# Kernel optimization log

Measured on AMD Instinct MI355X. Metric: run time of the kernel, lower is better.

## Reference

```python
import jax, jax.numpy as jnp
import numpy as np

N_PLAYERS, N_POS, N_TEAMS = 200000, 320, 32
FEAT, EMB, HID = 128, 64, 128
E_P2P, E_P2T, E_CHEM = 400000, 640, 1000000
NUM_ROUNDS = 3


def _linear(x, w, b):
    return x @ w + b


def _attention(emb, edges, q_w, q_b, k_w, k_b, v_w, v_b):
    # chemistry attention: softmax over ALL edges (dim=0 in the torch code)
    src, dst = edges[0], edges[1]
    Q = _linear(emb[dst], q_w, q_b)          # (E, EMB)
    K = _linear(emb[src], k_w, k_b)
    V = _linear(emb[src], v_w, v_b)
    scores = (Q * K).sum(axis=1) / jnp.asarray(EMB ** 0.5, emb.dtype)  # (E,)
    attn = jax.nn.softmax(scores)            # global softmax across edges
    messages = attn[:, None] * V             # (E, EMB)
    agg = jax.ops.segment_sum(messages, dst, num_segments=emb.shape[0])
    return emb + agg


def _message_pass(src_emb, dst_emb, edges, msg_w, msg_b, upd_w, upd_b):
    src, dst = edges[0], edges[1]
    messages = jax.nn.relu(_linear(src_emb[src], msg_w, msg_b))  # (E, EMB)
    n_dst = dst_emb.shape[0]
    agg = jax.ops.segment_sum(messages, dst, num_segments=n_dst)
    counts = jax.ops.segment_sum(jnp.ones((edges.shape[1],), src_emb.dtype), dst, num_segments=n_dst)
    agg = agg / jnp.clip(counts, 1.0)[:, None]  # mean aggregation
    h = jnp.concatenate([dst_emb, agg], axis=1)  # (n_dst, 2*EMB)
    return jax.nn.relu(_linear(h, upd_w, upd_b))


def setup_inputs() -> dict:
    key = jax.random.key(0)
    ks = jax.random.split(key, 32)
    g = lambda k, shape, fan_in: jax.random.normal(k, shape, jnp.float32) / np.sqrt(fan_in)
    inp = {}
    inp['player_features'] = jax.random.normal(ks[0], (N_PLAYERS, FEAT), jnp.float32)
    inp['position_indices'] = jax.random.randint(ks[1], (N_POS,), 0, 10, jnp.int32)
    inp['team_indices'] = jnp.arange(N_TEAMS, dtype=jnp.int32)
    inp['p2p_edges'] = jnp.stack([
        jax.random.randint(ks[2], (E_P2P,), 0, N_PLAYERS, jnp.int32),
        jax.random.randint(ks[3], (E_P2P,), 0, N_POS, jnp.int32)])
    inp['p2t_edges'] = jnp.stack([
        jax.random.randint(ks[4], (E_P2T,), 0, N_POS, jnp.int32),
        jax.random.randint(ks[5], (E_P2T,), 0, N_TEAMS, jnp.int32)])
    inp['chem_edges'] = jax.random.randint(ks[6], (2, E_CHEM), 0, N_PLAYERS, jnp.int32)
    inp['home_team_idx'] = 0
    inp['away_team_idx'] = 1
    # player encoder
    inp['enc_w1'] = g(ks[7], (FEAT, HID), FEAT); inp['enc_b1'] = jnp.zeros((HID,), jnp.float32)
    inp['enc_w2'] = g(ks[8], (HID, EMB), HID); inp['enc_b2'] = jnp.zeros((EMB,), jnp.float32)
    # embedding tables
    inp['pos_emb_table'] = jax.random.normal(ks[9], (10, EMB), jnp.float32)
    inp['team_emb_table'] = jax.random.normal(ks[10], (32, EMB), jnp.float32)
    # chemistry attention
    for name, k in (('q', ks[11]), ('k', ks[12]), ('v', ks[13])):
        inp[name + '_w'] = g(k, (EMB, EMB), EMB); inp[name + '_b'] = jnp.zeros((EMB,), jnp.float32)
    # message passing layers
    inp['p2p_msg_w'] = g(ks[14], (EMB, EMB), EMB); inp['p2p_msg_b'] = jnp.zeros((EMB,), jnp.float32)
    inp['p2p_upd_w'] = g(ks[15], (2 * EMB, EMB), 2 * EMB); inp['p2p_upd_b'] = jnp.zeros((EMB,), jnp.float32)
    inp['p2t_msg_w'] = g(ks[16], (EMB, EMB), EMB); inp['p2t_msg_b'] = jnp.zeros((EMB,), jnp.float32)
    inp['p2t_upd_w'] = g(ks[17], (2 * EMB, EMB), 2 * EMB); inp['p2t_upd_b'] = jnp.zeros((EMB,), jnp.float32)
    # game predictor
    inp['gp_w1'] = g(ks[18], (2 * EMB, HID), 2 * EMB); inp['gp_b1'] = jnp.zeros((HID,), jnp.float32)
    inp['gp_w2'] = g(ks[19], (HID, 64), HID); inp['gp_b2'] = jnp.zeros((64,), jnp.float32)
    inp['gp_w3'] = g(ks[20], (64, 1), 64); inp['gp_b3'] = jnp.zeros((1,), jnp.float32)
    return inp


def reference(player_features, position_indices, team_indices, p2p_edges, p2t_edges,
              chem_edges, home_team_idx, away_team_idx,
              enc_w1, enc_b1, enc_w2, enc_b2, pos_emb_table, team_emb_table,
              q_w, q_b, k_w, k_b, v_w, v_b,
              p2p_msg_w, p2p_msg_b, p2p_upd_w, p2p_upd_b,
              p2t_msg_w, p2t_msg_b, p2t_upd_w, p2t_upd_b,
              gp_w1, gp_b1, gp_w2, gp_b2, gp_w3, gp_b3):
    # player encoder (dropout omitted: eval mode)
    h = jax.nn.relu(_linear(player_features, enc_w1, enc_b1))
    player_embeds = _linear(h, enc_w2, enc_b2)  # (N_PLAYERS, EMB)
    player_embeds = _attention(player_embeds, chem_edges, q_w, q_b, k_w, k_b, v_w, v_b)
    position_embeds = pos_emb_table[position_indices]  # (N_POS, EMB)
    for _ in range(NUM_ROUNDS):
        position_embeds = _message_pass(player_embeds, position_embeds, p2p_edges,
                                        p2p_msg_w, p2p_msg_b, p2p_upd_w, p2p_upd_b)
    team_embeds = team_emb_table[team_indices]  # (N_TEAMS, EMB)
    for _ in range(NUM_ROUNDS):
        team_embeds = _message_pass(position_embeds, team_embeds, p2t_edges,
                                    p2t_msg_w, p2t_msg_b, p2t_upd_w, p2t_upd_b)
    game_embed = jnp.concatenate([team_embeds[home_team_idx], team_embeds[away_team_idx]])  # (2*EMB,)
    z = jax.nn.relu(_linear(game_embed, gp_w1, gp_b1))
    z = jax.nn.relu(_linear(z, gp_w2, gp_b2))
    logit = _linear(z, gp_w3, gp_b3)  # (1,)
    return jax.nn.sigmoid(logit)
```

## Files before the change

### kernel.cpp

```cpp
#include <hip/hip_runtime.h>
#include <hip/hip_bf16.h>

#define NP     200000
#define NPOS   320
#define NT     32
#define FEAT   128
#define EMB    64
#define HID    128
#define EP2P   400000
#define EP2T   640
#define ECHEM  1000000

#define CHEM_CAP 32
#define P2P_CAP  2048
#define T2_CAP   64
#define SC_GRID  2048
#define PB_BLOCKS 64
#define AGG_SPLIT 8

typedef unsigned short u16;
typedef __attribute__((ext_vector_type(8))) short short8;
typedef __attribute__((ext_vector_type(4))) float f32x4;

static __device__ inline u16 f2bf(float f) {
    unsigned u = __float_as_uint(f);
    return (u16)((u + 0x7fffu + ((u >> 16) & 1u)) >> 16);
}
static __device__ inline float bf2f(u16 h) {
    return __uint_as_float(((unsigned)h) << 16);
}
static __device__ inline float bprod(unsigned a, unsigned b) {
    float a0 = __uint_as_float(a << 16), a1 = __uint_as_float(a & 0xffff0000u);
    float b0 = __uint_as_float(b << 16), b1 = __uint_as_float(b & 0xffff0000u);
    return fmaf(a0, b0, a1 * b1);
}

__global__ __launch_bounds__(256) void init_kernel(int* __restrict__ chem_cnt,
                                                   int* __restrict__ p2p_cnt,
                                                   float* __restrict__ Zp,
                                                   const int* __restrict__ pos_idx,
                                                   const float* __restrict__ pos_table,
                                                   float* __restrict__ pos0,
                                                   float* __restrict__ pos_agg,
                                                   const float* __restrict__ w1,
                                                   const float* __restrict__ w2,
                                                   const float* __restrict__ qw,
                                                   const float* __restrict__ kw,
                                                   const float* __restrict__ vw,
                                                   const float* __restrict__ mw,
                                                   u16* __restrict__ Wpack)
{
    int t = blockIdx.x * 256 + threadIdx.x;
    if (t < NP) chem_cnt[t] = 0;
    if (t < NPOS) p2p_cnt[t] = 0;
    if (t < NPOS * EMB) {
        pos0[t] = pos_table[pos_idx[t >> 6] * EMB + (t & 63)];
        pos_agg[t] = 0.f;
    }
    if (t == 0) *Zp = 0.f;
    if (t < 40960) {
        float v;
        if (t < 16384)        { int i = t;         v = w1[(i & 127) * 128 + (i >> 7)]; }
        else if (t < 24576)   { int i = t - 16384; v = w2[(i & 127) * 64  + (i >> 7)]; }
        else if (t < 28672)   { int i = t - 24576; v = qw[(i & 63) * 64 + (i >> 6)]; }
        else if (t < 32768)   { int i = t - 28672; v = kw[(i & 63) * 64 + (i >> 6)]; }
        else if (t < 36864)   { int i = t - 32768; v = vw[(i & 63) * 64 + (i >> 6)]; }
        else                  { int i = t - 36864; v = mw[(i & 63) * 64 + (i >> 6)]; }
        Wpack[t] = f2bf(v);
    }
}

__global__ __launch_bounds__(256) void mfma_enc(
    const float* __restrict__ X,
    const u16* __restrict__ W1t, const u16* __restrict__ W2t,
    const u16* __restrict__ Qt,  const u16* __restrict__ Kt, const u16* __restrict__ Vt,
    const float* __restrict__ b1, const float* __restrict__ b2,
    const float* __restrict__ qbv, const float* __restrict__ kbv, const float* __restrict__ vbv,
    float* __restrict__ emb,
    u16* __restrict__ Qb, u16* __restrict__ Kb, u16* __restrict__ Vb)
{
    __shared__ u16 hb[4][16 * 136];
    __shared__ u16 eb[4][16 * 72];
    const int tid = threadIdx.x, wave = tid >> 6, lane = tid & 63;
    const int m_ = lane & 15, quad = lane >> 4;
    const int rbase = blockIdx.x * 64 + wave * 16;

    const float4* xrow = (const float4*)(X + (size_t)(rbase + m_) * 128);
    short8 ax[4];
#pragma unroll
    for (int kk = 0; kk < 4; ++kk) {
        float4 u = xrow[kk * 8 + quad * 2];
        float4 v = xrow[kk * 8 + quad * 2 + 1];
        short8 t;
        t[0] = (short)f2bf(u.x); t[1] = (short)f2bf(u.y);
        t[2] = (short)f2bf(u.z); t[3] = (short)f2bf(u.w);
        t[4] = (short)f2bf(v.x); t[5] = (short)f2bf(v.y);
        t[6] = (short)f2bf(v.z); t[7] = (short)f2bf(v.w);
        ax[kk] = t;
    }

    u16* hrow = &hb[wave][0];
#pragma unroll
    for (int n0 = 0; n0 < 8; ++n0) {
        float bv = b1[n0 * 16 + m_];
        f32x4 acc = {bv, bv, bv, bv};
        const short8* w = (const short8*)(W1t + (size_t)(n0 * 16 + m_) * 128);
#pragma unroll
        for (int kk = 0; kk < 4; ++kk)
            acc = __builtin_amdgcn_mfma_f32_16x16x32_bf16(ax[kk], w[kk * 4 + quad], acc, 0, 0, 0);
#pragma unroll
        for (int r = 0; r < 4; ++r)
            hrow[(quad * 4 + r) * 136 + n0 * 16 + m_] = f2bf(fmaxf(acc[r], 0.f));
    }

    short8 ah[4];
#pragma unroll
    for (int kk = 0; kk < 4; ++kk)
        ah[kk] = *(const short8*)&hrow[m_ * 136 + kk * 32 + quad * 8];

    u16* erow = &eb[wave][0];
#pragma unroll
    for (int n0 = 0; n0 < 4; ++n0) {
        float bv = b2[n0 * 16 + m_];
        f32x4 acc = {bv, bv, bv, bv};
        const short8* w = (const short8*)(W2t + (size_t)(n0 * 16 + m_) * 128);
#pragma unroll
        for (int kk = 0; kk < 4; ++kk)
            acc = __builtin_amdgcn_mfma_f32_16x16x32_bf16(ah[kk], w[kk * 4 + quad], acc, 0, 0, 0);
#pragma unroll
        for (int r = 0; r < 4; ++r) {
            float v = acc[r];
            emb[(size_t)(rbase + quad * 4 + r) * 64 + n0 * 16 + m_] = v;
            erow[(quad * 4 + r) * 72 + n0 * 16 + m_] = f2bf(v);
        }
    }

    short8 ae[2];
#pragma unroll
    for (int kk = 0; kk < 2; ++kk)
        ae[kk] = *(const short8*)&erow[m_ * 72 + kk * 32 + quad * 8];

    const u16*   Wt3[3] = {Qt, Kt, Vt};
    const float* Bb3[3] = {qbv, kbv, vbv};
    u16*         Ob3[3] = {Qb, Kb, Vb};
#pragma unroll
    for (int m3 = 0; m3 < 3; ++m3) {
        const u16* Wt = Wt3[m3];
        const float* bp = Bb3[m3];
        u16* O = Ob3[m3];
#pragma unroll
        for (int n0 = 0; n0 < 4; ++n0) {
            float bv = bp[n0 * 16 + m_];
            f32x4 acc = {bv, bv, bv, bv};
            const short8* w = (const short8*)(Wt + (size_t)(n0 * 16 + m_) * 64);
#pragma unroll
            for (int kk = 0; kk < 2; ++kk)
                acc = __builtin_amdgcn_mfma_f32_16x16x32_bf16(ae[kk], w[kk * 4 + quad], acc, 0, 0, 0);
#pragma unroll
            for (int r = 0; r < 4; ++r)
                O[(size_t)(rbase + quad * 4 + r) * 64 + n0 * 16 + m_] = f2bf(acc[r]);
        }
    }
}

__global__ __launch_bounds__(256) void chem_attn(const u16* __restrict__ Qb,
                                                 const u16* __restrict__ Kb,
                                                 const int* __restrict__ chem,
                                                 int* __restrict__ cnt,
                                                 uint2* __restrict__ swlist,
                                                 float* __restrict__ Zp)
{
    __shared__ float wsum[4];
    int tid = threadIdx.x;
    int lane = tid & 63, wave = tid >> 6;
    float zsum = 0.f;
    for (int e = blockIdx.x * 256 + tid; e < ECHEM; e += SC_GRID * 256) {
        int src = chem[e];
        int dst = chem[ECHEM + e];
        const uint4* q = (const uint4*)(Qb + (size_t)dst * 64);
        const uint4* k = (const uint4*)(Kb + (size_t)src * 64);
        uint4 qv[8], kv[8];
#pragma unroll
        for (int i = 0; i < 8; ++i) qv[i] = q[i];
#pragma unroll
        for (int i = 0; i < 8; ++i) kv[i] = k[i];
        float p = 0.f;
#pragma unroll
        for (int i = 0; i < 8; ++i)
            p += bprod(qv[i].x, kv[i].x) + bprod(qv[i].y, kv[i].y)
               + bprod(qv[i].z, kv[i].z) + bprod(qv[i].w, kv[i].w);
        float w = __expf(p * 0.125f);
        zsum += w;
        int pos = atomicAdd(&cnt[dst], 1);
        if (pos < CHEM_CAP)
            swlist[dst * CHEM_CAP + pos] = make_uint2((unsigned)src, __float_as_uint(w));
    }
    for (int off = 1; off < 64; off <<= 1) zsum += __shfl_xor(zsum, off);
    if (lane == 0) wsum[wave] = zsum;
    __syncthreads();
    if (tid == 0) atomicAdd(Zp, wsum[0] + wsum[1] + wsum[2] + wsum[3]);
}

__global__ __launch_bounds__(256) void chem_agg_msg(const float* __restrict__ emb,
                                                    const u16* __restrict__ Vb,
                                                    const int* __restrict__ cnt,
                                                    const uint2* __restrict__ swlist,
                                                    const float* __restrict__ Zp,
                                                    const u16* __restrict__ Msgt,
                                                    const float* __restrict__ mb,
                                                    u16* __restrict__ Mpb)
{
    __shared__ u16 eb[4][16 * 72];
    const int tid = threadIdx.x, wave = tid >> 6, lane = tid & 63;
    const int m_ = lane & 15, quad = lane >> 4;
    const int d0 = blockIdx.x * 64 + wave * 16;
    const int srow = lane >> 3, scol = (lane & 7) * 8;
    const float invZ = 1.f / Zp[0];
    u16* erow = &eb[wave][0];
#pragma unroll 1
    for (int t = 0; t < 16; ++t) {
        int d = d0 + t;
        float base = emb[(size_t)d * 64 + lane];
        int c = cnt[d]; if (c > CHEM_CAP) c = CHEM_CAP;
        int sv = 0; float wv = 0.f;
        if (lane < c) {
            uint2 p = swlist[d * CHEM_CAP + lane];
            sv = (int)p.x; wv = __uint_as_float(p.y);
        }
        float acc = 0.f;
        int i = 0;
        for (; i + 4 <= c; i += 4) {
            int s0 = __shfl(sv, i),     s1 = __shfl(sv, i + 1);
            int s2 = __shfl(sv, i + 2), s3 = __shfl(sv, i + 3);
            float w0 = __shfl(wv, i),     w1 = __shfl(wv, i + 1);
            float w2 = __shfl(wv, i + 2), w3 = __shfl(wv, i + 3);
            float v0 = bf2f(Vb[(size_t)s0 * 64 + lane]);
            float v1 = bf2f(Vb[(size_t)s1 * 64 + lane]);
            float v2 = bf2f(Vb[(size_t)s2 * 64 + lane]);
            float v3 = bf2f(Vb[(size_t)s3 * 64 + lane]);
            acc += w0 * v0 + w1 * v1 + w2 * v2 + w3 * v3;
        }
        for (; i < c; ++i) {
            int s = __shfl(sv, i);
            float w = __shfl(wv, i);
            acc += w * bf2f(Vb[(size_t)s * 64 + lane]);
        }
        erow[t * 72 + lane] = f2bf(base + acc * invZ);
    }
    short8 a0 = *(const short8*)&erow[m_ * 72 + quad * 8];
    short8 a1 = *(const short8*)&erow[m_ * 72 + 32 + quad * 8];
#pragma unroll
    for (int n0 = 0; n0 < 4; ++n0) {
        float bv = mb[n0 * 16 + m_];
        f32x4 acc = {bv, bv, bv, bv};
        const short8* w = (const short8*)(Msgt + (size_t)(n0 * 16 + m_) * 64);
        acc = __builtin_amdgcn_mfma_f32_16x16x32_bf16(a0, w[quad], acc, 0, 0, 0);
        acc = __builtin_amdgcn_mfma_f32_16x16x32_bf16(a1, w[4 + quad], acc, 0, 0, 0);
#pragma unroll
        for (int r = 0; r < 4; ++r)
            erow[(quad * 4 + r) * 72 + n0 * 16 + m_] = f2bf(fmaxf(acc[r], 0.f));
    }
    short8 r0 = *(const short8*)&erow[srow * 72 + scol];
    short8 r1 = *(const short8*)&erow[(srow + 8) * 72 + scol];
    *(short8*)(Mpb + (size_t)(d0 + srow) * 64 + scol) = r0;
    *(short8*)(Mpb + (size_t)(d0 + 8 + srow) * 64 + scol) = r1;
}

__global__ __launch_bounds__(256) void p2p_bucket(const int* __restrict__ p2p,
                                                  int* __restrict__ cnt,
                                                  int* __restrict__ list)
{
    __shared__ int lhist[NPOS];
    __shared__ int lbase[NPOS];
    int tid = threadIdx.x;
    for (int i = tid; i < NPOS; i += 256) lhist[i] = 0;
    __syncthreads();
    const int chunk = (EP2P + PB_BLOCKS - 1) / PB_BLOCKS;
    int e0 = blockIdx.x * chunk;
    int e1 = e0 + chunk; if (e1 > EP2P) e1 = EP2P;
    for (int e = e0 + tid; e < e1; e += 256)
        atomicAdd(&lhist[p2p[EP2P + e]], 1);
    __syncthreads();
    for (int i = tid; i < NPOS; i += 256) {
        lbase[i] = atomicAdd(&cnt[i], lhist[i]);
        lhist[i] = 0;
    }
    __syncthreads();
    for (int e = e0 + tid; e < e1; e += 256) {
        int d = p2p[EP2P + e];
        int p = lbase[d] + atomicAdd(&lhist[d], 1);
        if (p < P2P_CAP) list[d * P2P_CAP + p] = p2p[e];
    }
}

__global__ __launch_bounds__(256) void p2p_agg(const u16* __restrict__ Mpb,
                                               const int* __restrict__ cnt,
                                               const int* __restrict__ list,
                                               float* __restrict__ pos_agg)
{
    __shared__ float part[4 * 64];
    int d = blockIdx.x >> 3;
    int sp = blockIdx.x & (AGG_SPLIT - 1);
    int wave = threadIdx.x >> 6, lane = threadIdx.x & 63;
    int c = cnt[d];
    int cl = c > P2P_CAP ? P2P_CAP : c;
    int seg = (cl + AGG_SPLIT - 1) / AGG_SPLIT;
    int i0b = sp * seg;
    int i1 = i0b + seg; if (i1 > cl) i1 = cl;
    float acc = 0.f;
    for (int i0 = i0b + wave * 64; i0 < i1; i0 += 256) {
        int n = i1 - i0; if (n > 64) n = 64;
        int sv = (lane < n) ? list[d * P2P_CAP + i0 + lane] : 0;
        int i = 0;
        for (; i + 4 <= n; i += 4) {
            int s0 = __shfl(sv, i),     s1 = __shfl(sv, i + 1);
            int s2 = __shfl(sv, i + 2), s3 = __shfl(sv, i + 3);
            float v0 = bf2f(Mpb[(size_t)s0 * 64 + lane]);
            float v1 = bf2f(Mpb[(size_t)s1 * 64 + lane]);
            float v2 = bf2f(Mpb[(size_t)s2 * 64 + lane]);
            float v3 = bf2f(Mpb[(size_t)s3 * 64 + lane]);
            acc += v0 + v1 + v2 + v3;
        }
        for (; i < n; ++i) {
            int s = __shfl(sv, i);
            acc += bf2f(Mpb[(size_t)s * 64 + lane]);
        }
    }
    part[wave * 64 + lane] = acc;
    __syncthreads();
    if (wave == 0) {
        float t = part[lane] + part[64 + lane] + part[128 + lane] + part[192 + lane];
        atomicAdd(&pos_agg[d * 64 + lane], t);
    }
}

__global__ __launch_bounds__(256) void pos_rounds(const float* __restrict__ pos0,
                                                  const float* __restrict__ agg,
                                                  const int* __restrict__ cnt,
                                                  const float* __restrict__ upd_w,
                                                  const float* __restrict__ upd_b,
                                                  const float* __restrict__ msg_w,
                                                  const float* __restrict__ msg_b,
                                                  float* __restrict__ Mt)
{
    __shared__ float cur[4][64], nxt[4][64], aggw[4][64];
    int tid = threadIdx.x;
    int r = tid >> 6, j = tid & 63;
    int row = blockIdx.x * 4 + r;
    int c = cnt[row];
    float invc = 1.f / (float)(c < 1 ? 1 : c);
    float aw = 0.f;
    const float* ar = agg + row * 64;
#pragma unroll 8
    for (int k = 0; k < 64; ++k) aw += ar[k] * upd_w[(64 + k) * 64 + j];
    aggw[r][j] = aw * invc + upd_b[j];
    cur[r][j] = pos0[row * 64 + j];
    __syncthreads();
#pragma unroll 1
    for (int round = 0; round < 3; ++round) {
        float acc = aggw[r][j];
#pragma unroll 8
        for (int k = 0; k < 64; ++k) acc += cur[r][k] * upd_w[k * 64 + j];
        nxt[r][j] = fmaxf(acc, 0.f);
        __syncthreads();
        cur[r][j] = nxt[r][j];
        __syncthreads();
    }
    float acc = msg_b[j];
#pragma unroll 8
    for (int k = 0; k < 64; ++k) acc += cur[r][k] * msg_w[k * 64 + j];
    Mt[row * 64 + j] = fmaxf(acc, 0.f);
}

__global__ __launch_bounds__(256) void p2t_head(
    const float* __restrict__ Mt,
    const int* __restrict__ p2t_edges,
    const float* __restrict__ upd_w, const float* __restrict__ upd_b,
    const int* __restrict__ team_indices,
    const float* __restrict__ team_table,
    const int* __restrict__ home_p, const int* __restrict__ away_p,
    const float* __restrict__ gp_w1, const float* __restrict__ gp_b1,
    const float* __restrict__ gp_w2, const float* __restrict__ gp_b2,
    const float* __restrict__ gp_w3, const float* __restrict__ gp_b3,
    float* __restrict__ out)
{
    __shared__ int   tcnt[NT];
    __shared__ int   tlist[NT * T2_CAP];
    __shared__ float aggbar[NT * 64];
    __shared__ float teamA[NT * 64];
    __shared__ float teamB[NT * 64];
    __shared__ float z1[128];
    __shared__ float z2[64];
    int tid = threadIdx.x;

    if (tid < NT) tcnt[tid] = 0;
    __syncthreads();
    for (int e = tid; e < EP2T; e += 256) {
        int s = p2t_edges[e], d = p2t_edges[EP2T + e];
        int p = atomicAdd(&tcnt[d], 1);
        if (p < T2_CAP) tlist[d * T2_CAP + p] = s;
    }
    __syncthreads();
    for (int i = tid; i < NT * 64; i += 256) {
        int d = i >> 6, c = i & 63;
        int cn = tcnt[d];
        int cl = cn > T2_CAP ? T2_CAP : cn;
        float acc = 0.f;
        for (int j = 0; j < cl; ++j) acc += Mt[tlist[d * T2_CAP + j] * 64 + c];
        float dv = cn < 1 ? 1.f : (float)cn;
        aggbar[i] = acc / dv;
        teamA[i] = team_table[team_indices[d] * 64 + c];
    }
    __syncthreads();

    float* tin = teamA; float* tout = teamB;
    for (int round = 0; round < 3; ++round) {
        for (int i = tid; i < NT * 64; i += 256) {
            int r = i >> 6, j = i & 63;
            float acc = upd_b[j];
            for (int k = 0; k < 64; ++k) acc += tin[r * 64 + k] * upd_w[k * 64 + j];
            for (int k = 0; k < 64; ++k) acc += aggbar[r * 64 + k] * upd_w[(64 + k) * 64 + j];
            tout[i] = fmaxf(acc, 0.f);
        }
        __syncthreads();
        float* tmp = tin; tin = tout; tout = tmp;
    }

    int home = home_p[0], away = away_p[0];
    if (tid < 128) {
        float acc = gp_b1[tid];
        for (int k = 0; k < 128; ++k) {
            float g = (k < 64) ? tin[home * 64 + k] : tin[away * 64 + (k - 64)];
            acc += g * gp_w1[k * 128 + tid];
        }
        z1[tid] = fmaxf(acc, 0.f);
    }
    __syncthreads();
    if (tid < 64) {
        float acc = gp_b2[tid];
        for (int k = 0; k < 128; ++k) acc += z1[k] * gp_w2[k * 64 + tid];
        z2[tid] = fmaxf(acc, 0.f);
    }
    __syncthreads();
    if (tid == 0) {
        float acc = gp_b3[0];
        for (int k = 0; k < 64; ++k) acc += z2[k] * gp_w3[k];
        out[0] = 1.f / (1.f + __expf(-acc));
    }
}

extern "C" void kernel_launch(void* const* d_in, const int* in_sizes, int n_in,
                              void* d_out, int out_size, void* d_ws, size_t ws_size,
                              hipStream_t stream)
{
    const float* X        = (const float*)d_in[0];
    const int*   pos_idx  = (const int*)d_in[1];
    const int*   team_idx = (const int*)d_in[2];
    const int*   p2p      = (const int*)d_in[3];
    const int*   p2t      = (const int*)d_in[4];
    const int*   chem     = (const int*)d_in[5];
    const int*   home_p   = (const int*)d_in[6];
    const int*   away_p   = (const int*)d_in[7];
    const float* enc_w1   = (const float*)d_in[8];
    const float* enc_b1   = (const float*)d_in[9];
    const float* enc_w2   = (const float*)d_in[10];
    const float* enc_b2   = (const float*)d_in[11];
    const float* pos_tab  = (const float*)d_in[12];
    const float* team_tab = (const float*)d_in[13];
    const float* q_w = (const float*)d_in[14]; const float* q_b = (const float*)d_in[15];
    const float* k_w = (const float*)d_in[16]; const float* k_b = (const float*)d_in[17];
    const float* v_w = (const float*)d_in[18]; const float* v_b = (const float*)d_in[19];
    const float* p2p_msg_w = (const float*)d_in[20]; const float* p2p_msg_b = (const float*)d_in[21];
    const float* p2p_upd_w = (const float*)d_in[22]; const float* p2p_upd_b = (const float*)d_in[23];
    const float* p2t_msg_w = (const float*)d_in[24]; const float* p2t_msg_b = (const float*)d_in[25];
    const float* p2t_upd_w = (const float*)d_in[26]; const float* p2t_upd_b = (const float*)d_in[27];
    const float* gp_w1 = (const float*)d_in[28]; const float* gp_b1 = (const float*)d_in[29];
    const float* gp_w2 = (const float*)d_in[30]; const float* gp_b2 = (const float*)d_in[31];
    const float* gp_w3 = (const float*)d_in[32]; const float* gp_b3 = (const float*)d_in[33];
    float* out = (float*)d_out;

    char* ws = (char*)d_ws;
    uint2*    swlist    = (uint2*)(ws + 0);
    float*    emb       = (float*)(ws + 51200000);
    u16*      Qb        = (u16*)  (ws + 102400000);
    u16*      Kb        = (u16*)  (ws + 128000000);
    u16*      Vb        = (u16*)  (ws + 153600000);
    u16*      Mpb       = (u16*)  (ws + 179200000);
    int*      p2p_list  = (int*)  (ws + 204800000);
    int*      chem_cnt  = (int*)  (ws + 207421440);
    int*      p2p_cnt   = (int*)  (ws + 208221440);
    float*    pos_agg   = (float*)(ws + 208222720);
    float*    posA      = (float*)(ws + 208304640);
    float*    Mt        = (float*)(ws + 208386560);
    float*    Zp        = (float*)(ws + 208468480);
    u16*      Wpack     = (u16*)  (ws + 208468496);
    u16* W1t  = Wpack;
    u16* W2t  = Wpack + 16384;
    u16* Qt   = Wpack + 24576;
    u16* Kt   = Wpack + 28672;
    u16* Vt   = Wpack + 32768;
    u16* Msgt = Wpack + 36864;

    const int NB_NP = (NP + 255) / 256;

    hipLaunchKernelGGL(init_kernel, dim3(NB_NP), dim3(256), 0, stream,
                       chem_cnt, p2p_cnt, Zp, pos_idx, pos_tab, posA, pos_agg,
                       enc_w1, enc_w2, q_w, k_w, v_w, p2p_msg_w, Wpack);
    hipLaunchKernelGGL(mfma_enc, dim3(NP / 64), dim3(256), 0, stream,
                       X, W1t, W2t, Qt, Kt, Vt,
                       enc_b1, enc_b2, q_b, k_b, v_b,
                       emb, Qb, Kb, Vb);
    hipLaunchKernelGGL(chem_attn, dim3(SC_GRID), dim3(256), 0, stream,
                       Qb, Kb, chem, chem_cnt, swlist, Zp);
    hipLaunchKernelGGL(chem_agg_msg, dim3(NP / 64), dim3(256), 0, stream,
                       emb, Vb, chem_cnt, swlist, Zp, Msgt, p2p_msg_b, Mpb);
    hipLaunchKernelGGL(p2p_bucket, dim3(PB_BLOCKS), dim3(256), 0, stream, p2p, p2p_cnt, p2p_list);
    hipLaunchKernelGGL(p2p_agg, dim3(NPOS * AGG_SPLIT), dim3(256), 0, stream,
                       Mpb, p2p_cnt, p2p_list, pos_agg);
    hipLaunchKernelGGL(pos_rounds, dim3(NPOS / 4), dim3(256), 0, stream,
                       posA, pos_agg, p2p_cnt, p2p_upd_w, p2p_upd_b,
                       p2t_msg_w, p2t_msg_b, Mt);
    hipLaunchKernelGGL(p2t_head, dim3(1), dim3(256), 0, stream,
                       Mt, p2t, p2t_upd_w, p2t_upd_b, team_idx, team_tab, home_p, away_p,
                       gp_w1, gp_b1, gp_w2, gp_b2, gp_w3, gp_b3, out);
}
```

Baseline: 619.6 us.

## Restructure chemistry attention into dst-bucketed gather with fused unnormalized aggregation

Chemistry edges are now bucketed by destination in a separate pass before the encoder. A per-destination wave kernel then computes the Q·K scores, the exp weights and the weighted V sum in one gather, writing an unnormalized aggregate and a per-node partition sum. A small reduction kernel produces the global softmax denominator, and the final message kernel only rescales. The encoder also becomes a persistent grid-stride kernel that prefetches the next chunk's inputs into registers. This avoids writing and re-reading weighted edge lists and the per-edge scattered K loads, at the cost of extra kernel launches, wider per-lane gathers and a bf16 rounding of the intermediate aggregate.

```diff
diff --git a/kernel.cpp b/kernel.cpp
--- a/kernel.cpp
+++ b/kernel.cpp
@@ -17,6 +17,8 @@
 #define SC_GRID  2048
 #define PB_BLOCKS 64
 #define AGG_SPLIT 8
+#define ENC_GRID 1024
+#define NCHUNK   (NP / 64)
 
 typedef unsigned short u16;
 typedef __attribute__((ext_vector_type(8))) short short8;
@@ -28,11 +30,6 @@
 }
 static __device__ inline float bf2f(u16 h) {
     return __uint_as_float(((unsigned)h) << 16);
-}
-static __device__ inline float bprod(unsigned a, unsigned b) {
-    float a0 = __uint_as_float(a << 16), a1 = __uint_as_float(a & 0xffff0000u);
-    float b0 = __uint_as_float(b << 16), b1 = __uint_as_float(b & 0xffff0000u);
-    return fmaf(a0, b0, a1 * b1);
 }
 
 __global__ __launch_bounds__(256) void init_kernel(int* __restrict__ chem_cnt,
@@ -83,128 +80,194 @@
     __shared__ u16 eb[4][16 * 72];
     const int tid = threadIdx.x, wave = tid >> 6, lane = tid & 63;
     const int m_ = lane & 15, quad = lane >> 4;
-    const int rbase = blockIdx.x * 64 + wave * 16;
-
-    const float4* xrow = (const float4*)(X + (size_t)(rbase + m_) * 128);
-    short8 ax[4];
-#pragma unroll
-    for (int kk = 0; kk < 4; ++kk) {
-        float4 u = xrow[kk * 8 + quad * 2];
-        float4 v = xrow[kk * 8 + quad * 2 + 1];
-        short8 t;
-        t[0] = (short)f2bf(u.x); t[1] = (short)f2bf(u.y);
-        t[2] = (short)f2bf(u.z); t[3] = (short)f2bf(u.w);
-        t[4] = (short)f2bf(v.x); t[5] = (short)f2bf(v.y);
-        t[6] = (short)f2bf(v.z); t[7] = (short)f2bf(v.w);
-        ax[kk] = t;
-    }
-
-    u16* hrow = &hb[wave][0];
-#pragma unroll
-    for (int n0 = 0; n0 < 8; ++n0) {
-        float bv = b1[n0 * 16 + m_];
-        f32x4 acc = {bv, bv, bv, bv};
-        const short8* w = (const short8*)(W1t + (size_t)(n0 * 16 + m_) * 128);
+
+    int chunk = blockIdx.x;
+    if (chunk >= NCHUNK) return;
+
+    float4 cur[8];
+    {
+        const float4* xr = (const float4*)(X + (size_t)(chunk * 64 + wave * 16 + m_) * 128);
+#pragma unroll
+        for (int kk = 0; kk < 4; ++kk) {
+            cur[2 * kk]     = xr[kk * 8 + quad * 2];
+            cur[2 * kk + 1] = xr[kk * 8 + quad * 2 + 1];
+        }
+    }
+
+    while (true) {
+        int nextc = chunk + ENC_GRID;
+        bool has_next = nextc < NCHUNK;
+        float4 nxt[8];
+        if (has_next) {
+            const float4* xr = (const float4*)(X + (size_t)(nextc * 64 + wave * 16 + m_) * 128);
+#pragma unroll
+            for (int kk = 0; kk < 4; ++kk) {
+                nxt[2 * kk]     = xr[kk * 8 + quad * 2];
+                nxt[2 * kk + 1] = xr[kk * 8 + quad * 2 + 1];
+            }
+        }
+
+        const int rbase = chunk * 64 + wave * 16;
+        short8 ax[4];
+#pragma unroll
+        for (int kk = 0; kk < 4; ++kk) {
+            float4 u = cur[2 * kk], v = cur[2 * kk + 1];
+            short8 t;
+            t[0] = (short)f2bf(u.x); t[1] = (short)f2bf(u.y);
+            t[2] = (short)f2bf(u.z); t[3] = (short)f2bf(u.w);
+            t[4] = (short)f2bf(v.x); t[5] = (short)f2bf(v.y);
+            t[6] = (short)f2bf(v.z); t[7] = (short)f2bf(v.w);
+            ax[kk] = t;
+        }
+
+        u16* hrow = &hb[wave][0];
+#pragma unroll
+        for (int n0 = 0; n0 < 8; ++n0) {
+            float bv = b1[n0 * 16 + m_];
+            f32x4 acc = {bv, bv, bv, bv};
+            const short8* w = (const short8*)(W1t + (size_t)(n0 * 16 + m_) * 128);
+#pragma unroll
+            for (int kk = 0; kk < 4; ++kk)
+                acc = __builtin_amdgcn_mfma_f32_16x16x32_bf16(ax[kk], w[kk * 4 + quad], acc, 0, 0, 0);
+#pragma unroll
+            for (int r = 0; r < 4; ++r)
+                hrow[(quad * 4 + r) * 136 + n0 * 16 + m_] = f2bf(fmaxf(acc[r], 0.f));
+        }
+
+        short8 ah[4];
 #pragma unroll
         for (int kk = 0; kk < 4; ++kk)
-            acc = __builtin_amdgcn_mfma_f32_16x16x32_bf16(ax[kk], w[kk * 4 + quad], acc, 0, 0, 0);
-#pragma unroll
-        for (int r = 0; r < 4; ++r)
-            hrow[(quad * 4 + r) * 136 + n0 * 16 + m_] = f2bf(fmaxf(acc[r], 0.f));
-    }
-
-    short8 ah[4];
-#pragma unroll
-    for (int kk = 0; kk < 4; ++kk)
-        ah[kk] = *(const short8*)&hrow[m_ * 136 + kk * 32 + quad * 8];
-
-    u16* erow = &eb[wave][0];
-#pragma unroll
-    for (int n0 = 0; n0 < 4; ++n0) {
-        float bv = b2[n0 * 16 + m_];
-        f32x4 acc = {bv, bv, bv, bv};
-        const short8* w = (const short8*)(W2t + (size_t)(n0 * 16 + m_) * 128);
-#pragma unroll
-        for (int kk = 0; kk < 4; ++kk)
-            acc = __builtin_amdgcn_mfma_f32_16x16x32_bf16(ah[kk], w[kk * 4 + quad], acc, 0, 0, 0);
-#pragma unroll
-        for (int r = 0; r < 4; ++r) {
-            float v = acc[r];
-            emb[(size_t)(rbase + quad * 4 + r) * 64 + n0 * 16 + m_] = v;
-            erow[(quad * 4 + r) * 72 + n0 * 16 + m_] = f2bf(v);
-        }
-    }
-
-    short8 ae[2];
-#pragma unroll
-    for (int kk = 0; kk < 2; ++kk)
-        ae[kk] = *(const short8*)&erow[m_ * 72 + kk * 32 + quad * 8];
-
-    const u16*   Wt3[3] = {Qt, Kt, Vt};
-    const float* Bb3[3] = {qbv, kbv, vbv};
-    u16*         Ob3[3] = {Qb, Kb, Vb};
-#pragma unroll
-    for (int m3 = 0; m3 < 3; ++m3) {
-        const u16* Wt = Wt3[m3];
-        const float* bp = Bb3[m3];
-        u16* O = Ob3[m3];
+            ah[kk] = *(const short8*)&hrow[m_ * 136 + kk * 32 + quad * 8];
+
+        u16* erow = &eb[wave][0];
 #pragma unroll
         for (int n0 = 0; n0 < 4; ++n0) {
-            float bv = bp[n0 * 16 + m_];
+            float bv = b2[n0 * 16 + m_];
             f32x4 acc = {bv, bv, bv, bv};
-            const short8* w = (const short8*)(Wt + (size_t)(n0 * 16 + m_) * 64);
-#pragma unroll
-            for (int kk = 0; kk < 2; ++kk)
-                acc = __builtin_amdgcn_mfma_f32_16x16x32_bf16(ae[kk], w[kk * 4 + quad], acc, 0, 0, 0);
-#pragma unroll
-            for (int r = 0; r < 4; ++r)
-                O[(size_t)(rbase + quad * 4 + r) * 64 + n0 * 16 + m_] = f2bf(acc[r]);
-        }
-    }
-}
-
-__global__ __launch_bounds__(256) void chem_attn(const u16* __restrict__ Qb,
+            const short8* w = (const short8*)(W2t + (size_t)(n0 * 16 + m_) * 128);
+#pragma unroll
+            for (int kk = 0; kk < 4; ++kk)
+                acc = __builtin_amdgcn_mfma_f32_16x16x32_bf16(ah[kk], w[kk * 4 + quad], acc, 0, 0, 0);
+#pragma unroll
+            for (int r = 0; r < 4; ++r) {
+                float v = acc[r];
+                emb[(size_t)(rbase + quad * 4 + r) * 64 + n0 * 16 + m_] = v;
+                erow[(quad * 4 + r) * 72 + n0 * 16 + m_] = f2bf(v);
+            }
+        }
+
+        short8 ae[2];
+#pragma unroll
+        for (int kk = 0; kk < 2; ++kk)
+            ae[kk] = *(const short8*)&erow[m_ * 72 + kk * 32 + quad * 8];
+
+        const u16*   Wt3[3] = {Qt, Kt, Vt};
+        const float* Bb3[3] = {qbv, kbv, vbv};
+        u16*         Ob3[3] = {Qb, Kb, Vb};
+#pragma unroll
+        for (int m3 = 0; m3 < 3; ++m3) {
+            const u16* Wt = Wt3[m3];
+            const float* bp = Bb3[m3];
+            u16* O = Ob3[m3];
+#pragma unroll
+            for (int n0 = 0; n0 < 4; ++n0) {
+                float bv = bp[n0 * 16 + m_];
+                f32x4 acc = {bv, bv, bv, bv};
+                const short8* w = (const short8*)(Wt + (size_t)(n0 * 16 + m_) * 64);
+#pragma unroll
+                for (int kk = 0; kk < 2; ++kk)
+                    acc = __builtin_amdgcn_mfma_f32_16x16x32_bf16(ae[kk], w[kk * 4 + quad], acc, 0, 0, 0);
+#pragma unroll
+                for (int r = 0; r < 4; ++r)
+                    O[(size_t)(rbase + quad * 4 + r) * 64 + n0 * 16 + m_] = f2bf(acc[r]);
+            }
+        }
+
+        if (!has_next) break;
+#pragma unroll
+        for (int i = 0; i < 8; ++i) cur[i] = nxt[i];
+        chunk = nextc;
+    }
+}
+
+__global__ __launch_bounds__(256) void chem_bucket(const int* __restrict__ chem,
+                                                   int* __restrict__ cnt,
+                                                   int* __restrict__ slist)
+{
+    for (int e = blockIdx.x * 256 + threadIdx.x; e < ECHEM; e += SC_GRID * 256) {
+        int d = chem[ECHEM + e];
+        int s = chem[e];
+        int pos = atomicAdd(&cnt[d], 1);
+        if (pos < CHEM_CAP) slist[d * CHEM_CAP + pos] = s;
+    }
+}
+
+__global__ __launch_bounds__(256) void chem_wsum(const u16* __restrict__ Qb,
                                                  const u16* __restrict__ Kb,
-                                                 const int* __restrict__ chem,
-                                                 int* __restrict__ cnt,
-                                                 uint2* __restrict__ swlist,
-                                                 float* __restrict__ Zp)
+                                                 const u16* __restrict__ Vb,
+                                                 const int* __restrict__ cnt,
+                                                 const int* __restrict__ slist,
+                                                 u16* __restrict__ T,
+                                                 float* __restrict__ Zd)
+{
+    const int wave = threadIdx.x >> 6, lane = threadIdx.x & 63;
+    const int d0 = blockIdx.x * 16 + wave * 4;
+#pragma unroll 1
+    for (int t = 0; t < 4; ++t) {
+        int d = d0 + t;
+        int c = cnt[d]; if (c > CHEM_CAP) c = CHEM_CAP;
+        float q = bf2f(Qb[(size_t)d * 64 + lane]);
+        int sv = (lane < c) ? slist[d * CHEM_CAP + lane] : 0;
+        float accT = 0.f, zd = 0.f;
+        int i = 0;
+        for (; i + 2 <= c; i += 2) {
+            int s0 = __shfl(sv, i), s1 = __shfl(sv, i + 1);
+            float k0 = bf2f(Kb[(size_t)s0 * 64 + lane]);
+            float v0 = bf2f(Vb[(size_t)s0 * 64 + lane]);
+            float k1 = bf2f(Kb[(size_t)s1 * 64 + lane]);
+            float v1 = bf2f(Vb[(size_t)s1 * 64 + lane]);
+            float p0 = q * k0, p1 = q * k1;
+            p0 += __shfl_xor(p0, 1);  p1 += __shfl_xor(p1, 1);
+            p0 += __shfl_xor(p0, 2);  p1 += __shfl_xor(p1, 2);
+            p0 += __shfl_xor(p0, 4);  p1 += __shfl_xor(p1, 4);
+            p0 += __shfl_xor(p0, 8);  p1 += __shfl_xor(p1, 8);
+            p0 += __shfl_xor(p0, 16); p1 += __shfl_xor(p1, 16);
+            p0 += __shfl_xor(p0, 32); p1 += __shfl_xor(p1, 32);
+            float w0 = __expf(p0 * 0.125f), w1 = __expf(p1 * 0.125f);
+            zd += w0 + w1;
+            accT += w0 * v0 + w1 * v1;
+        }
+        if (i < c) {
+            int s = __shfl(sv, i);
+            float kc = bf2f(Kb[(size_t)s * 64 + lane]);
+            float vc = bf2f(Vb[(size_t)s * 64 + lane]);
+            float p = q * kc;
+            p += __shfl_xor(p, 1);  p += __shfl_xor(p, 2);
+            p += __shfl_xor(p, 4);  p += __shfl_xor(p, 8);
+            p += __shfl_xor(p, 16); p += __shfl_xor(p, 32);
+            float w = __expf(p * 0.125f);
+            zd += w; accT += w * vc;
+        }
+        T[(size_t)d * 64 + lane] = f2bf(accT);
+        if (lane == 0) Zd[d] = zd;
+    }
+}
+
+__global__ __launch_bounds__(256) void zred(const float* __restrict__ Zd,
+                                            float* __restrict__ Zp)
 {
     __shared__ float wsum[4];
-    int tid = threadIdx.x;
-    int lane = tid & 63, wave = tid >> 6;
-    float zsum = 0.f;
-    for (int e = blockIdx.x * 256 + tid; e < ECHEM; e += SC_GRID * 256) {
-        int src = chem[e];
-        int dst = chem[ECHEM + e];
-        const uint4* q = (const uint4*)(Qb + (size_t)dst * 64);
-        const uint4* k = (const uint4*)(Kb + (size_t)src * 64);
-        uint4 qv[8], kv[8];
-#pragma unroll
-        for (int i = 0; i < 8; ++i) qv[i] = q[i];
-#pragma unroll
-        for (int i = 0; i < 8; ++i) kv[i] = k[i];
-        float p = 0.f;
-#pragma unroll
-        for (int i = 0; i < 8; ++i)
-            p += bprod(qv[i].x, kv[i].x) + bprod(qv[i].y, kv[i].y)
-               + bprod(qv[i].z, kv[i].z) + bprod(qv[i].w, kv[i].w);
-        float w = __expf(p * 0.125f);
-        zsum += w;
-        int pos = atomicAdd(&cnt[dst], 1);
-        if (pos < CHEM_CAP)
-            swlist[dst * CHEM_CAP + pos] = make_uint2((unsigned)src, __float_as_uint(w));
-    }
-    for (int off = 1; off < 64; off <<= 1) zsum += __shfl_xor(zsum, off);
-    if (lane == 0) wsum[wave] = zsum;
-    __syncthreads();
-    if (tid == 0) atomicAdd(Zp, wsum[0] + wsum[1] + wsum[2] + wsum[3]);
-}
-
-__global__ __launch_bounds__(256) void chem_agg_msg(const float* __restrict__ emb,
-                                                    const u16* __restrict__ Vb,
-                                                    const int* __restrict__ cnt,
-                                                    const uint2* __restrict__ swlist,
+    float s = 0.f;
+    for (int i = blockIdx.x * 256 + threadIdx.x; i < NP; i += 256 * 256)
+        s += Zd[i];
+    for (int off = 1; off < 64; off <<= 1) s += __shfl_xor(s, off);
+    if ((threadIdx.x & 63) == 0) wsum[threadIdx.x >> 6] = s;
+    __syncthreads();
+    if (threadIdx.x == 0) atomicAdd(Zp, wsum[0] + wsum[1] + wsum[2] + wsum[3]);
+}
+
+__global__ __launch_bounds__(256) void chem_fin_msg(const float* __restrict__ emb,
+                                                    const u16* __restrict__ T,
                                                     const float* __restrict__ Zp,
                                                     const u16* __restrict__ Msgt,
                                                     const float* __restrict__ mb,
@@ -217,35 +280,11 @@
     const int srow = lane >> 3, scol = (lane & 7) * 8;
     const float invZ = 1.f / Zp[0];
     u16* erow = &eb[wave][0];
-#pragma unroll 1
+#pragma unroll
     for (int t = 0; t < 16; ++t) {
         int d = d0 + t;
-        float base = emb[(size_t)d * 64 + lane];
-        int c = cnt[d]; if (c > CHEM_CAP) c = CHEM_CAP;
-        int sv = 0; float wv = 0.f;
-        if (lane < c) {
-            uint2 p = swlist[d * CHEM_CAP + lane];
-            sv = (int)p.x; wv = __uint_as_float(p.y);
-        }
-        float acc = 0.f;
-        int i = 0;
-        for (; i + 4 <= c; i += 4) {
-            int s0 = __shfl(sv, i),     s1 = __shfl(sv, i + 1);
-            int s2 = __shfl(sv, i + 2), s3 = __shfl(sv, i + 3);
-            float w0 = __shfl(wv, i),     w1 = __shfl(wv, i + 1);
-            float w2 = __shfl(wv, i + 2), w3 = __shfl(wv, i + 3);
-            float v0 = bf2f(Vb[(size_t)s0 * 64 + lane]);
-            float v1 = bf2f(Vb[(size_t)s1 * 64 + lane]);
-            float v2 = bf2f(Vb[(size_t)s2 * 64 + lane]);
-            float v3 = bf2f(Vb[(size_t)s3 * 64 + lane]);
-            acc += w0 * v0 + w1 * v1 + w2 * v2 + w3 * v3;
-        }
-        for (; i < c; ++i) {
-            int s = __shfl(sv, i);
-            float w = __shfl(wv, i);
-            acc += w * bf2f(Vb[(size_t)s * 64 + lane]);
-        }
-        erow[t * 72 + lane] = f2bf(base + acc * invZ);
+        float v = emb[(size_t)d * 64 + lane] + bf2f(T[(size_t)d * 64 + lane]) * invZ;
+        erow[t * 72 + lane] = f2bf(v);
     }
     short8 a0 = *(const short8*)&erow[m_ * 72 + quad * 8];
     short8 a1 = *(const short8*)&erow[m_ * 72 + 32 + quad * 8];
@@ -480,7 +519,8 @@
     float* out = (float*)d_out;
 
     char* ws = (char*)d_ws;
-    uint2*    swlist    = (uint2*)(ws + 0);
+    int*      slist     = (int*)  (ws + 0);
+    u16*      T         = (u16*)  (ws + 25600000);
     float*    emb       = (float*)(ws + 51200000);
     u16*      Qb        = (u16*)  (ws + 102400000);
     u16*      Kb        = (u16*)  (ws + 128000000);
@@ -488,12 +528,13 @@
     u16*      Mpb       = (u16*)  (ws + 179200000);
     int*      p2p_list  = (int*)  (ws + 204800000);
     int*      chem_cnt  = (int*)  (ws + 207421440);
-    int*      p2p_cnt   = (int*)  (ws + 208221440);
-    float*    pos_agg   = (float*)(ws + 208222720);
-    float*    posA      = (float*)(ws + 208304640);
-    float*    Mt        = (float*)(ws + 208386560);
-    float*    Zp        = (float*)(ws + 208468480);
-    u16*      Wpack     = (u16*)  (ws + 208468496);
+    float*    Zd        = (float*)(ws + 208221440);
+    int*      p2p_cnt   = (int*)  (ws + 209021440);
+    float*    pos_agg   = (float*)(ws + 209022720);
+    float*    posA      = (float*)(ws + 209104640);
+    float*    Mt        = (float*)(ws + 209186560);
+    float*    Zp        = (float*)(ws + 209268480);
+    u16*      Wpack     = (u16*)  (ws + 209268496);
     u16* W1t  = Wpack;
     u16* W2t  = Wpack + 16384;
     u16* Qt   = Wpack + 24576;
@@ -506,14 +547,16 @@
     hipLaunchKernelGGL(init_kernel, dim3(NB_NP), dim3(256), 0, stream,
                        chem_cnt, p2p_cnt, Zp, pos_idx, pos_tab, posA, pos_agg,
                        enc_w1, enc_w2, q_w, k_w, v_w, p2p_msg_w, Wpack);
-    hipLaunchKernelGGL(mfma_enc, dim3(NP / 64), dim3(256), 0, stream,
+    hipLaunchKernelGGL(chem_bucket, dim3(SC_GRID), dim3(256), 0, stream, chem, chem_cnt, slist);
+    hipLaunchKernelGGL(mfma_enc, dim3(ENC_GRID), dim3(256), 0, stream,
                        X, W1t, W2t, Qt, Kt, Vt,
                        enc_b1, enc_b2, q_b, k_b, v_b,
                        emb, Qb, Kb, Vb);
-    hipLaunchKernelGGL(chem_attn, dim3(SC_GRID), dim3(256), 0, stream,
-                       Qb, Kb, chem, chem_cnt, swlist, Zp);
-    hipLaunchKernelGGL(chem_agg_msg, dim3(NP / 64), dim3(256), 0, stream,
-                       emb, Vb, chem_cnt, swlist, Zp, Msgt, p2p_msg_b, Mpb);
+    hipLaunchKernelGGL(chem_wsum, dim3(NP / 16), dim3(256), 0, stream,
+                       Qb, Kb, Vb, chem_cnt, slist, T, Zd);
+    hipLaunchKernelGGL(zred, dim3(256), dim3(256), 0, stream, Zd, Zp);
+    hipLaunchKernelGGL(chem_fin_msg, dim3(NP / 64), dim3(256), 0, stream,
+                       emb, T, Zp, Msgt, p2p_msg_b, Mpb);
     hipLaunchKernelGGL(p2p_bucket, dim3(PB_BLOCKS), dim3(256), 0, stream, p2p, p2p_cnt, p2p_list);
     hipLaunchKernelGGL(p2p_agg, dim3(NPOS * AGG_SPLIT), dim3(256), 0, stream,
                        Mpb, p2p_cnt, p2p_list, pos_agg);
```

Result: faster. 593.2 us (-4.3%).
